# Kernel optimization log

Measured on AMD Instinct MI355X. Metric: run time of the kernel, lower is better.

## Reference

```python
import jax, jax.numpy as jnp
import numpy as np

N_WIRES = 8
DIM = 1 << N_WIRES  # 256

# --- static precompute: CNOT-ring basis permutation and PauliZ sign matrix ---
# torchquantum convention: wire 0 is the most significant bit of the basis index.
_gates = [(w, w + 1) for w in range(N_WIRES - 1)] + [(N_WIRES - 1, 0)]
_perm = np.empty(DIM, dtype=np.int64)
for b in range(DIM):
    bits = [(b >> (N_WIRES - 1 - w)) & 1 for w in range(N_WIRES)]
    for c, t in _gates:
        if bits[c]:
            bits[t] ^= 1
    _perm[b] = sum(bit << (N_WIRES - 1 - w) for w, bit in enumerate(bits))
_Z = np.array([[1.0 - 2.0 * ((idx >> (N_WIRES - 1 - w)) & 1) for w in range(N_WIRES)]
               for idx in range(DIM)], dtype=np.float32)
# exp_Z[w] = sum_b probs_in[b] * Z[perm[b], w]  (CNOTs permute basis states)
_M = jnp.asarray(_Z[_perm])  # [256, 8]


def _quantum_head(angles):
    """angles: [..., 8] RX angles -> PauliZ expectations [..., 8].

    Circuit: RX(angle_w) on each wire from |0>, CNOT ring, MeasureAll(PauliZ).
    Post-RX state is a product state; CNOTs only permute basis states, so
    probabilities suffice (no complex amplitudes needed).
    """
    half = angles * 0.5
    c2 = jnp.cos(half) ** 2  # P(qubit=0)
    s2 = jnp.sin(half) ** 2  # P(qubit=1)
    # Build the 256-dim joint probability vector via sequential outer products.
    p = jnp.ones(angles.shape[:-1] + (1,), angles.dtype)
    for w in range(N_WIRES):
        pw = jnp.stack([c2[..., w], s2[..., w]], axis=-1)  # [..., 2]
        p = (p[..., :, None] * pw[..., None, :]).reshape(angles.shape[:-1] + (-1,))
    return p @ _M.astype(p.dtype)  # [..., 8]


def setup_inputs() -> dict:
    key = jax.random.key(0)
    ks = jax.random.split(key, 6)
    B, S, E = 8, 512, 768
    scale = 1.0 / np.sqrt(E)
    return {
        "x": jax.random.normal(ks[0], (B, S, E), jnp.float32),
        "W_proj": jax.random.normal(ks[1], (E, E), jnp.float32) * scale,
        "b_proj": jax.random.normal(ks[2], (E,), jnp.float32) * 0.02,
        "theta": jax.random.normal(ks[3], (N_WIRES,), jnp.float32),
        "W_comb": jax.random.normal(ks[4], (E, E), jnp.float32) * scale,
        "b_comb": jax.random.normal(ks[5], (E,), jnp.float32) * 0.02,
    }


def reference(x, W_proj, b_proj, theta, W_comb, b_comb):
    B, S, E = x.shape
    H = E // N_WIRES  # num_heads = 96
    proj = x @ W_proj.T + b_proj                 # [B, S, E] (torch Linear)
    angles = proj.reshape(B, S, H, N_WIRES) + theta  # encoder RX(x) then RX(theta): angles add
    expz = _quantum_head(angles)                 # [B, S, H, 8]
    out = expz.reshape(B, S, E)                  # heads re-concatenated
    # dropout is identity in eval mode
    return out @ W_comb.T + b_comb
```

## Files before the change

kernel.cpp:

```cpp
#include <hip/hip_runtime.h>

typedef _Float16 v8h __attribute__((ext_vector_type(8)));
typedef float    v4f __attribute__((ext_vector_type(4)));

__device__ __forceinline__ void gl_lds16(const void* g, void* l) {
  __builtin_amdgcn_global_load_lds(
      (__attribute__((address_space(1))) void*)(void*)g,
      (__attribute__((address_space(3))) void*)l, 16, 0, 0);
}
__device__ __forceinline__ v8h cvt8(const float4 a, const float4 b) {
  v8h o;
  o[0] = (_Float16)a.x; o[1] = (_Float16)a.y; o[2] = (_Float16)a.z; o[3] = (_Float16)a.w;
  o[4] = (_Float16)b.x; o[5] = (_Float16)b.y; o[6] = (_Float16)b.z; o[7] = (_Float16)b.w;
  return o;
}

__global__ void conv_w(const float4* __restrict__ wp, const float4* __restrict__ wc,
                       v8h* __restrict__ op, v8h* __restrict__ oc) {
  const int n = 73728;
  int i = blockIdx.x * blockDim.x + threadIdx.x;
  const float4* src = (i < n) ? wp : wc;
  v8h* dst = (i < n) ? op : oc;
  const int j = (i < n) ? i : i - n;
  dst[j] = cvt8(src[2 * j], src[2 * j + 1]);
}


__global__ __launch_bounds__(256) void gemm1_qh(
    const float* __restrict__ X,
    const _Float16* __restrict__ B,
    const float* __restrict__ bp,
    const float* __restrict__ theta,
    _Float16* __restrict__ EZ) {
  const int t = threadIdx.x;
  const int b = blockIdx.x;
  const int xcd = b & 7, slot = b >> 3;
  const int bm = xcd * 8 + slot / 12;
  const int bn = slot % 12;

  const int wave = t >> 6, lane = t & 63;
  const int quad = lane >> 4, l16 = lane & 15;
  const int wm = (wave >> 1) * 32, wn = (wave & 1) * 32;

  __shared__ __align__(16) unsigned char smem[32768];
  _Float16* As = (_Float16*)smem;
  _Float16* Bs = (_Float16*)(smem + 16384);
  float* Cs = (float*)smem;

  const float4 th0 = *(const float4*)theta;
  const float4 th1 = *(const float4*)(theta + 4);

  const int tr = t >> 4;
  const int tc = t & 15;
  const int cgl = tc ^ tr;

  const float*    Xg = X + (size_t)(bm * 64 + tr) * 768 + cgl * 8;
  const _Float16* Bg = B + (size_t)(bn * 64 + tr) * 768 + cgl * 8;

  v4f acc[2][2];
#pragma unroll
  for (int i = 0; i < 2; i++)
#pragma unroll
    for (int j = 0; j < 2; j++) acc[i][j] = (v4f){0.f, 0.f, 0.f, 0.f};

  float4 xr[4][2];
#pragma unroll
  for (int c = 0; c < 4; c++) {
    const float* p = Xg + (size_t)c * 16 * 768;
    xr[c][0] = *(const float4*)p;
    xr[c][1] = *(const float4*)(p + 4);
  }

  for (int kt = 0; kt < 768; kt += 128) {
#pragma unroll
    for (int c = 0; c < 4; c++)
      gl_lds16(Bg + (size_t)c * 16 * 768 + kt, &Bs[c * 2048 + t * 8]);
#pragma unroll
    for (int c = 0; c < 4; c++)
      *(v8h*)&As[c * 2048 + t * 8] = cvt8(xr[c][0], xr[c][1]);
    __syncthreads();
    if (kt + 128 < 768) {
#pragma unroll
      for (int c = 0; c < 4; c++) {
        const float* p = Xg + (size_t)c * 16 * 768 + kt + 128;
        xr[c][0] = *(const float4*)p;
        xr[c][1] = *(const float4*)(p + 4);
      }
    }
#pragma unroll
    for (int q = 0; q < 4; q++) {
      v8h af[2], bf[2];
#pragma unroll
      for (int i = 0; i < 2; i++)
        af[i] = *(const v8h*)&As[(wm + i * 16 + l16) * 128 + (((q * 4 + quad) ^ l16) * 8)];
#pragma unroll
      for (int j = 0; j < 2; j++)
        bf[j] = *(const v8h*)&Bs[(wn + j * 16 + l16) * 128 + (((q * 4 + quad) ^ l16) * 8)];
#pragma unroll
      for (int i = 0; i < 2; i++)
#pragma unroll
        for (int j = 0; j < 2; j++)
          acc[i][j] = __builtin_amdgcn_mfma_f32_16x16x32_f16(af[i], bf[j], acc[i][j], 0, 0, 0);
    }
    __syncthreads();
  }

  const int r0 = wm + quad * 4;
  const int c0 = wn + l16;
#pragma unroll
  for (int j = 0; j < 2; j++)
#pragma unroll
    for (int i = 0; i < 2; i++)
#pragma unroll
      for (int r = 0; r < 4; r++)
        Cs[(r0 + i * 16 + r) * 68 + c0 + j * 16] = acc[i][j][r];
  __syncthreads();

#pragma unroll
  for (int s = 0; s < 2; s++) {
    const int idx = t + s * 256;
    const int row = idx >> 3, h = idx & 7;
    const int gcol = bn * 64 + h * 8;
    const float* cr = &Cs[row * 68 + h * 8];
    const float4 q0 = *(const float4*)cr;
    const float4 q1 = *(const float4*)(cr + 4);
    const float4 b0 = *(const float4*)(bp + gcol);
    const float4 b1 = *(const float4*)(bp + gcol + 4);
    float c[8];
    c[0] = cosf(q0.x + b0.x + th0.x);
    c[1] = cosf(q0.y + b0.y + th0.y);
    c[2] = cosf(q0.z + b0.z + th0.z);
    c[3] = cosf(q0.w + b0.w + th0.w);
    c[4] = cosf(q1.x + b1.x + th1.x);
    c[5] = cosf(q1.y + b1.y + th1.y);
    c[6] = cosf(q1.z + b1.z + th1.z);
    c[7] = cosf(q1.w + b1.w + th1.w);
    float e[8];
    e[0] = c[1] * c[2] * c[3] * c[4] * c[5] * c[6] * c[7];
    float pr = c[0];
#pragma unroll
    for (int w = 1; w < 8; w++) { pr *= c[w]; e[w] = pr; }
    v8h ov;
#pragma unroll
    for (int w = 0; w < 8; w++) ov[w] = (_Float16)e[w];
    *(v8h*)(EZ + (size_t)(bm * 64 + row) * 768 + gcol) = ov;
  }
}

__global__ __launch_bounds__(256) void gemm2(
    const _Float16* __restrict__ A,
    const _Float16* __restrict__ B,
    float* __restrict__ C,
    const float* __restrict__ bias) {
  const int t = threadIdx.x;
  const int b = blockIdx.x;
  const int xcd = b & 7, slot = b >> 3;
  const int bm = xcd * 8 + slot / 12;
  const int bn = slot % 12;

  const int wave = t >> 6, lane = t & 63;
  const int quad = lane >> 4, l16 = lane & 15;
  const int wm = (wave >> 1) * 32, wn = (wave & 1) * 32;

  __shared__ __align__(16) _Float16 As[64 * 128];
  __shared__ __align__(16) _Float16 Bs[64 * 128];

  const int tr = t >> 4;
  const int tc = t & 15;
  const int cgl = tc ^ tr;

  const _Float16* Ag = A + (size_t)(bm * 64 + tr) * 768 + cgl * 8;
  const _Float16* Bg = B + (size_t)(bn * 64 + tr) * 768 + cgl * 8;

  v4f acc[2][2];
#pragma unroll
  for (int i = 0; i < 2; i++)
#pragma unroll
    for (int j = 0; j < 2; j++) acc[i][j] = (v4f){0.f, 0.f, 0.f, 0.f};

  for (int kt = 0; kt < 768; kt += 128) {
#pragma unroll
    for (int c = 0; c < 4; c++) {
      gl_lds16(Ag + (size_t)c * 16 * 768 + kt, &As[c * 2048 + t * 8]);
      gl_lds16(Bg + (size_t)c * 16 * 768 + kt, &Bs[c * 2048 + t * 8]);
    }
    __syncthreads();
#pragma unroll
    for (int q = 0; q < 4; q++) {
      v8h af[2], bf[2];
#pragma unroll
      for (int i = 0; i < 2; i++)
        af[i] = *(const v8h*)&As[(wm + i * 16 + l16) * 128 + (((q * 4 + quad) ^ l16) * 8)];
#pragma unroll
      for (int j = 0; j < 2; j++)
        bf[j] = *(const v8h*)&Bs[(wn + j * 16 + l16) * 128 + (((q * 4 + quad) ^ l16) * 8)];
#pragma unroll
      for (int ii = 0; ii < 2; ii++)
#pragma unroll
        for (int j = 0; j < 2; j++)
          acc[ii][j] = __builtin_amdgcn_mfma_f32_16x16x32_f16(af[ii], bf[j], acc[ii][j], 0, 0, 0);
    }
    __syncthreads();
  }

  const int row0 = bm * 64 + wm + quad * 4;
  const int col0 = bn * 64 + wn + l16;
#pragma unroll
  for (int j = 0; j < 2; j++) {
    const int col = col0 + j * 16;
    const float bv = bias[col];
#pragma unroll
    for (int i = 0; i < 2; i++) {
#pragma unroll
      for (int r = 0; r < 4; r++) {
        C[(size_t)(row0 + i * 16 + r) * 768 + col] = acc[i][j][r] + bv;
      }
    }
  }
}

extern "C" void kernel_launch(void* const* d_in, const int* in_sizes, int n_in,
                              void* d_out, int out_size, void* d_ws, size_t ws_size,
                              hipStream_t stream) {
  const float* x     = (const float*)d_in[0];
  const float* Wp    = (const float*)d_in[1];
  const float* bp    = (const float*)d_in[2];
  const float* theta = (const float*)d_in[3];
  const float* Wcf   = (const float*)d_in[4];
  const float* bc    = (const float*)d_in[5];
  float* out = (float*)d_out;

  const size_t EE = (size_t)768 * 768;

  _Float16* WPH = (_Float16*)d_ws;
  _Float16* WCH = WPH + EE;
  _Float16* EZ  = WCH + EE;

  conv_w<<<(int)(2 * EE / 8 / 256), 256, 0, stream>>>(
      (const float4*)Wp, (const float4*)Wcf, (v8h*)WPH, (v8h*)WCH);

  gemm1_qh<<<768, 256, 0, stream>>>(x, WPH, bp, theta, EZ);

  gemm2<<<768, 256, 0, stream>>>(EZ, WCH, out, bc);
}
```

Before: 99.02 us.

## Fuse both GEMMs into one kernel with per-row-block flag synchronization

Merges the projection+quantum-head GEMM and the combine GEMM into a single persistent-style launch. Each block writes its EZ tile, increments a per-row-block counter, and spins until all 12 column blocks for that row block finish before running the second GEMM. This removes one kernel launch and the inter-kernel gap, at the cost of a memset, spin-waiting, and reliance on all 768 blocks being co-resident (launch bounds raised to 3 blocks per SM). If the blocks sharing a row block are not all resident, the guard counter times out and the second GEMM can read stale EZ data.

Measured after the change: 236.7 us. 2.39x slower.

```diff
diff --git a/kernel.cpp b/kernel.cpp
--- a/kernel.cpp
+++ b/kernel.cpp
@@ -25,13 +25,16 @@
   dst[j] = cvt8(src[2 * j], src[2 * j + 1]);
 }
 
-
-__global__ __launch_bounds__(256) void gemm1_qh(
+__global__ __launch_bounds__(256, 3) void fused_gemm(
     const float* __restrict__ X,
-    const _Float16* __restrict__ B,
+    const _Float16* __restrict__ WP,
+    const _Float16* __restrict__ WC,
     const float* __restrict__ bp,
     const float* __restrict__ theta,
-    _Float16* __restrict__ EZ) {
+    const float* __restrict__ bc,
+    _Float16* __restrict__ EZ,
+    float* __restrict__ OUT,
+    unsigned int* __restrict__ flags) {
   const int t = threadIdx.x;
   const int b = blockIdx.x;
   const int xcd = b & 7, slot = b >> 3;
@@ -47,173 +50,164 @@
   _Float16* Bs = (_Float16*)(smem + 16384);
   float* Cs = (float*)smem;
 
-  const float4 th0 = *(const float4*)theta;
-  const float4 th1 = *(const float4*)(theta + 4);
-
   const int tr = t >> 4;
   const int tc = t & 15;
   const int cgl = tc ^ tr;
 
-  const float*    Xg = X + (size_t)(bm * 64 + tr) * 768 + cgl * 8;
-  const _Float16* Bg = B + (size_t)(bn * 64 + tr) * 768 + cgl * 8;
-
-  v4f acc[2][2];
-#pragma unroll
-  for (int i = 0; i < 2; i++)
-#pragma unroll
-    for (int j = 0; j < 2; j++) acc[i][j] = (v4f){0.f, 0.f, 0.f, 0.f};
-
-  float4 xr[4][2];
-#pragma unroll
-  for (int c = 0; c < 4; c++) {
-    const float* p = Xg + (size_t)c * 16 * 768;
-    xr[c][0] = *(const float4*)p;
-    xr[c][1] = *(const float4*)(p + 4);
+  {
+    const float4 th0 = *(const float4*)theta;
+    const float4 th1 = *(const float4*)(theta + 4);
+
+    const float*    Xg = X + (size_t)(bm * 64 + tr) * 768 + cgl * 8;
+    const _Float16* Bg = WP + (size_t)(bn * 64 + tr) * 768 + cgl * 8;
+
+    v4f acc[2][2];
+#pragma unroll
+    for (int i = 0; i < 2; i++)
+#pragma unroll
+      for (int j = 0; j < 2; j++) acc[i][j] = (v4f){0.f, 0.f, 0.f, 0.f};
+
+    float4 xr[4][2];
+#pragma unroll
+    for (int c = 0; c < 4; c++) {
+      const float* p = Xg + (size_t)c * 16 * 768;
+      xr[c][0] = *(const float4*)p;
+      xr[c][1] = *(const float4*)(p + 4);
+    }
+
+    for (int kt = 0; kt < 768; kt += 128) {
+#pragma unroll
+      for (int c = 0; c < 4; c++)
+        gl_lds16(Bg + (size_t)c * 16 * 768 + kt, &Bs[c * 2048 + t * 8]);
+#pragma unroll
+      for (int c = 0; c < 4; c++)
+        *(v8h*)&As[c * 2048 + t * 8] = cvt8(xr[c][0], xr[c][1]);
+      __syncthreads();
+      if (kt + 128 < 768) {
+#pragma unroll
+        for (int c = 0; c < 4; c++) {
+          const float* p = Xg + (size_t)c * 16 * 768 + kt + 128;
+          xr[c][0] = *(const float4*)p;
+          xr[c][1] = *(const float4*)(p + 4);
+        }
+      }
+#pragma unroll
+      for (int q = 0; q < 4; q++) {
+        v8h af[2], bf[2];
+#pragma unroll
+        for (int i = 0; i < 2; i++)
+          af[i] = *(const v8h*)&As[(wm + i * 16 + l16) * 128 + (((q * 4 + quad) ^ l16) * 8)];
+#pragma unroll
+        for (int j = 0; j < 2; j++)
+          bf[j] = *(const v8h*)&Bs[(wn + j * 16 + l16) * 128 + (((q * 4 + quad) ^ l16) * 8)];
+#pragma unroll
+        for (int i = 0; i < 2; i++)
+#pragma unroll
+          for (int j = 0; j < 2; j++)
+            acc[i][j] = __builtin_amdgcn_mfma_f32_16x16x32_f16(af[i], bf[j], acc[i][j], 0, 0, 0);
+      }
+      __syncthreads();
+    }
+
+    const int r0 = wm + quad * 4;
+    const int c0 = wn + l16;
+#pragma unroll
+    for (int j = 0; j < 2; j++)
+#pragma unroll
+      for (int i = 0; i < 2; i++)
+#pragma unroll
+        for (int r = 0; r < 4; r++)
+          Cs[(r0 + i * 16 + r) * 68 + c0 + j * 16] = acc[i][j][r];
+    __syncthreads();
+
+#pragma unroll
+    for (int s = 0; s < 2; s++) {
+      const int idx = t + s * 256;
+      const int row = idx >> 3, h = idx & 7;
+      const int gcol = bn * 64 + h * 8;
+      const float* cr = &Cs[row * 68 + h * 8];
+      const float4 q0 = *(const float4*)cr;
+      const float4 q1 = *(const float4*)(cr + 4);
+      const float4 b0 = *(const float4*)(bp + gcol);
+      const float4 b1 = *(const float4*)(bp + gcol + 4);
+      float c[8];
+      c[0] = cosf(q0.x + b0.x + th0.x);
+      c[1] = cosf(q0.y + b0.y + th0.y);
+      c[2] = cosf(q0.z + b0.z + th0.z);
+      c[3] = cosf(q0.w + b0.w + th0.w);
+      c[4] = cosf(q1.x + b1.x + th1.x);
+      c[5] = cosf(q1.y + b1.y + th1.y);
+      c[6] = cosf(q1.z + b1.z + th1.z);
+      c[7] = cosf(q1.w + b1.w + th1.w);
+      float e[8];
+      e[0] = c[1] * c[2] * c[3] * c[4] * c[5] * c[6] * c[7];
+      float pr = c[0];
+#pragma unroll
+      for (int w = 1; w < 8; w++) { pr *= c[w]; e[w] = pr; }
+      v8h ov;
+#pragma unroll
+      for (int w = 0; w < 8; w++) ov[w] = (_Float16)e[w];
+      *(v8h*)(EZ + (size_t)(bm * 64 + row) * 768 + gcol) = ov;
+    }
   }
 
-  for (int kt = 0; kt < 768; kt += 128) {
-#pragma unroll
-    for (int c = 0; c < 4; c++)
-      gl_lds16(Bg + (size_t)c * 16 * 768 + kt, &Bs[c * 2048 + t * 8]);
-#pragma unroll
-    for (int c = 0; c < 4; c++)
-      *(v8h*)&As[c * 2048 + t * 8] = cvt8(xr[c][0], xr[c][1]);
-    __syncthreads();
-    if (kt + 128 < 768) {
+  __threadfence();
+  __syncthreads();
+  if (t == 0) atomicAdd(&flags[bm], 1u);
+  if (t == 0) {
+    unsigned int guard = 1u << 20;
+    while (atomicAdd(&flags[bm], 0u) < 12u && --guard) { }
+  }
+  __syncthreads();
+  __threadfence();
+
+  {
+    const _Float16* Ag = EZ + (size_t)(bm * 64 + tr) * 768 + cgl * 8;
+    const _Float16* Bg = WC + (size_t)(bn * 64 + tr) * 768 + cgl * 8;
+
+    v4f acc[2][2];
+#pragma unroll
+    for (int i = 0; i < 2; i++)
+#pragma unroll
+      for (int j = 0; j < 2; j++) acc[i][j] = (v4f){0.f, 0.f, 0.f, 0.f};
+
+    for (int kt = 0; kt < 768; kt += 128) {
 #pragma unroll
       for (int c = 0; c < 4; c++) {
-        const float* p = Xg + (size_t)c * 16 * 768 + kt + 128;
-        xr[c][0] = *(const float4*)p;
-        xr[c][1] = *(const float4*)(p + 4);
-      }
-    }
-#pragma unroll
-    for (int q = 0; q < 4; q++) {
-      v8h af[2], bf[2];
-#pragma unroll
-      for (int i = 0; i < 2; i++)
-        af[i] = *(const v8h*)&As[(wm + i * 16 + l16) * 128 + (((q * 4 + quad) ^ l16) * 8)];
-#pragma unroll
-      for (int j = 0; j < 2; j++)
-        bf[j] = *(const v8h*)&Bs[(wn + j * 16 + l16) * 128 + (((q * 4 + quad) ^ l16) * 8)];
-#pragma unroll
-      for (int i = 0; i < 2; i++)
+        gl_lds16(Ag + (size_t)c * 16 * 768 + kt, &As[c * 2048 + t * 8]);
+        gl_lds16(Bg + (size_t)c * 16 * 768 + kt, &Bs[c * 2048 + t * 8]);
+      }
+      __syncthreads();
+#pragma unroll
+      for (int q = 0; q < 4; q++) {
+        v8h af[2], bf[2];
+#pragma unroll
+        for (int i = 0; i < 2; i++)
+          af[i] = *(const v8h*)&As[(wm + i * 16 + l16) * 128 + (((q * 4 + quad) ^ l16) * 8)];
 #pragma unroll
         for (int j = 0; j < 2; j++)
-          acc[i][j] = __builtin_amdgcn_mfma_f32_16x16x32_f16(af[i], bf[j], acc[i][j], 0, 0, 0);
-    }
-    __syncthreads();
-  }
-
-  const int r0 = wm + quad * 4;
-  const int c0 = wn + l16;
-#pragma unroll
-  for (int j = 0; j < 2; j++)
-#pragma unroll
-    for (int i = 0; i < 2; i++)
-#pragma unroll
-      for (int r = 0; r < 4; r++)
-        Cs[(r0 + i * 16 + r) * 68 + c0 + j * 16] = acc[i][j][r];
-  __syncthreads();
-
-#pragma unroll
-  for (int s = 0; s < 2; s++) {
-    const int idx = t + s * 256;
-    const int row = idx >> 3, h = idx & 7;
-    const int gcol = bn * 64 + h * 8;
-    const float* cr = &Cs[row * 68 + h * 8];
-    const float4 q0 = *(const float4*)cr;
-    const float4 q1 = *(const float4*)(cr + 4);
-    const float4 b0 = *(const float4*)(bp + gcol);
-    const float4 b1 = *(const float4*)(bp + gcol + 4);
-    float c[8];
-    c[0] = cosf(q0.x + b0.x + th0.x);
-    c[1] = cosf(q0.y + b0.y + th0.y);
-    c[2] = cosf(q0.z + b0.z + th0.z);
-    c[3] = cosf(q0.w + b0.w + th0.w);
-    c[4] = cosf(q1.x + b1.x + th1.x);
-    c[5] = cosf(q1.y + b1.y + th1.y);
-    c[6] = cosf(q1.z + b1.z + th1.z);
-    c[7] = cosf(q1.w + b1.w + th1.w);
-    float e[8];
-    e[0] = c[1] * c[2] * c[3] * c[4] * c[5] * c[6] * c[7];
-    float pr = c[0];
-#pragma unroll
-    for (int w = 1; w < 8; w++) { pr *= c[w]; e[w] = pr; }
-    v8h ov;
-#pragma unroll
-    for (int w = 0; w < 8; w++) ov[w] = (_Float16)e[w];
-    *(v8h*)(EZ + (size_t)(bm * 64 + row) * 768 + gcol) = ov;
-  }
-}
-
-__global__ __launch_bounds__(256) void gemm2(
-    const _Float16* __restrict__ A,
-    const _Float16* __restrict__ B,
-    float* __restrict__ C,
-    const float* __restrict__ bias) {
-  const int t = threadIdx.x;
-  const int b = blockIdx.x;
-  const int xcd = b & 7, slot = b >> 3;
-  const int bm = xcd * 8 + slot / 12;
-  const int bn = slot % 12;
-
-  const int wave = t >> 6, lane = t & 63;
-  const int quad = lane >> 4, l16 = lane & 15;
-  const int wm = (wave >> 1) * 32, wn = (wave & 1) * 32;
-
-  __shared__ __align__(16) _Float16 As[64 * 128];
-  __shared__ __align__(16) _Float16 Bs[64 * 128];
-
-  const int tr = t >> 4;
-  const int tc = t & 15;
-  const int cgl = tc ^ tr;
-
-  const _Float16* Ag = A + (size_t)(bm * 64 + tr) * 768 + cgl * 8;
-  const _Float16* Bg = B + (size_t)(bn * 64 + tr) * 768 + cgl * 8;
-
-  v4f acc[2][2];
-#pragma unroll
-  for (int i = 0; i < 2; i++)
-#pragma unroll
-    for (int j = 0; j < 2; j++) acc[i][j] = (v4f){0.f, 0.f, 0.f, 0.f};
-
-  for (int kt = 0; kt < 768; kt += 128) {
-#pragma unroll
-    for (int c = 0; c < 4; c++) {
-      gl_lds16(Ag + (size_t)c * 16 * 768 + kt, &As[c * 2048 + t * 8]);
-      gl_lds16(Bg + (size_t)c * 16 * 768 + kt, &Bs[c * 2048 + t * 8]);
-    }
-    __syncthreads();
-#pragma unroll
-    for (int q = 0; q < 4; q++) {
-      v8h af[2], bf[2];
-#pragma unroll
-      for (int i = 0; i < 2; i++)
-        af[i] = *(const v8h*)&As[(wm + i * 16 + l16) * 128 + (((q * 4 + quad) ^ l16) * 8)];
-#pragma unroll
-      for (int j = 0; j < 2; j++)
-        bf[j] = *(const v8h*)&Bs[(wn + j * 16 + l16) * 128 + (((q * 4 + quad) ^ l16) * 8)];
-#pragma unroll
-      for (int ii = 0; ii < 2; ii++)
-#pragma unroll
-        for (int j = 0; j < 2; j++)
-          acc[ii][j] = __builtin_amdgcn_mfma_f32_16x16x32_f16(af[ii], bf[j], acc[ii][j], 0, 0, 0);
-    }
-    __syncthreads();
-  }
-
-  const int row0 = bm * 64 + wm + quad * 4;
-  const int col0 = bn * 64 + wn + l16;
-#pragma unroll
-  for (int j = 0; j < 2; j++) {
-    const int col = col0 + j * 16;
-    const float bv = bias[col];
-#pragma unroll
-    for (int i = 0; i < 2; i++) {
-#pragma unroll
-      for (int r = 0; r < 4; r++) {
-        C[(size_t)(row0 + i * 16 + r) * 768 + col] = acc[i][j][r] + bv;
+          bf[j] = *(const v8h*)&Bs[(wn + j * 16 + l16) * 128 + (((q * 4 + quad) ^ l16) * 8)];
+#pragma unroll
+        for (int ii = 0; ii < 2; ii++)
+#pragma unroll
+          for (int j = 0; j < 2; j++)
+            acc[ii][j] = __builtin_amdgcn_mfma_f32_16x16x32_f16(af[ii], bf[j], acc[ii][j], 0, 0, 0);
+      }
+      __syncthreads();
+    }
+
+    const int row0 = bm * 64 + wm + quad * 4;
+    const int col0 = bn * 64 + wn + l16;
+#pragma unroll
+    for (int j = 0; j < 2; j++) {
+      const int col = col0 + j * 16;
+      const float bv = bc[col];
+#pragma unroll
+      for (int i = 0; i < 2; i++) {
+#pragma unroll
+        for (int r = 0; r < 4; r++) {
+          OUT[(size_t)(row0 + i * 16 + r) * 768 + col] = acc[i][j][r] + bv;
+        }
       }
     }
   }
@@ -231,15 +225,17 @@
   float* out = (float*)d_out;
 
   const size_t EE = (size_t)768 * 768;
+  const size_t ME = (size_t)4096 * 768;
 
   _Float16* WPH = (_Float16*)d_ws;
   _Float16* WCH = WPH + EE;
   _Float16* EZ  = WCH + EE;
+  unsigned int* flags = (unsigned int*)(EZ + ME);
+
+  hipMemsetAsync(flags, 0, 64 * sizeof(unsigned int), stream);
 
   conv_w<<<(int)(2 * EE / 8 / 256), 256, 0, stream>>>(
       (const float4*)Wp, (const float4*)Wcf, (v8h*)WPH, (v8h*)WCH);
 
-  gemm1_qh<<<768, 256, 0, stream>>>(x, WPH, bp, theta, EZ);
-
-  gemm2<<<768, 256, 0, stream>>>(EZ, WCH, out, bc);
-}
+  fused_gemm<<<768, 256, 0, stream>>>(x, WPH, WCH, bp, theta, bc, EZ, out, flags);
+}
```
